# Performance work log

Hardware: AMD Instinct MI355X
Metric: run time of the kernel (lower is better)

Reference implementation:

```python
import jax, jax.numpy as jnp
import numpy as np

N_POINTS = 300000
N_PAIRS = 100000  # rulebook pairs per kernel offset
K_OFFSETS = 27    # 3x3x3 kernel
C_IN, C_OUT = 32, 64
GROUPS = 8
EPS = 1e-5
NEG_SLOPE = 0.01


def setup_inputs() -> dict:
    key = jax.random.key(0)
    k1, k2, k3, k4 = jax.random.split(key, 4)
    feats = jax.random.normal(k1, (N_POINTS, C_IN), dtype=jnp.float32)
    weight = jax.random.normal(k2, (K_OFFSETS, C_IN, C_OUT), dtype=jnp.float32) * (1.0 / np.sqrt(C_IN * K_OFFSETS))
    gamma = jnp.ones((C_OUT,), dtype=jnp.float32)
    beta = jnp.zeros((C_OUT,), dtype=jnp.float32)
    in_idx = jax.random.randint(k3, (K_OFFSETS, N_PAIRS), 0, N_POINTS, dtype=jnp.int64)
    out_idx = jax.random.randint(k4, (K_OFFSETS, N_PAIRS), 0, N_POINTS, dtype=jnp.int64)
    return {"feats": feats, "weight": weight, "gamma": gamma, "beta": beta,
            "in_idx": in_idx, "out_idx": out_idx}


def reference(feats, weight, gamma, beta, in_idx, out_idx):
    # Sparse 3D conv via rulebook: gather -> per-offset matmul -> scatter-add
    gathered = feats[in_idx]                       # [K, P, C_in]
    y = jnp.einsum('kpi,kio->kpo', gathered, weight)  # [K, P, C_out]
    out = jnp.zeros((feats.shape[0], weight.shape[2]), feats.dtype)
    out = out.at[out_idx.reshape(-1)].add(y.reshape(-1, weight.shape[2]))
    # GroupNorm(8, C_out): stats over all points and channels within each group
    N, C = out.shape
    xg = out.reshape(N, GROUPS, C // GROUPS)
    mean = jnp.mean(xg, axis=(0, 2), keepdims=True)
    var = jnp.var(xg, axis=(0, 2), keepdims=True)
    xn = ((xg - mean) * jax.lax.rsqrt(var + EPS)).reshape(N, C)
    xn = xn * gamma + beta
    # LeakyReLU (default negative_slope = 0.01)
    return jnp.where(xn >= 0, xn, NEG_SLOPE * xn)
```

## Files before the change

kernel.cpp:

```cpp
#include <hip/hip_runtime.h>

#define NPTS   300000
#define NPAIRS 100000
#define KOFF   27
#define CIN    32
#define COUT   64
#define NGROUP 8
#define EPSV   1e-5f
#define SLOPE  0.01f

#define PAIRS_PER_BLOCK 256
#define BLOCKS_PER_K ((NPAIRS + PAIRS_PER_BLOCK - 1) / PAIRS_PER_BLOCK)

__global__ __launch_bounds__(256) void zero_kernel(float4* __restrict__ out4, int n4,
                                                   float* __restrict__ stats) {
    int i = blockIdx.x * blockDim.x + threadIdx.x;
    if (i < n4) out4[i] = make_float4(0.f, 0.f, 0.f, 0.f);
    if (blockIdx.x == 0 && threadIdx.x < 16) stats[threadIdx.x] = 0.f;
}

__global__ __launch_bounds__(256) void conv_kernel(
    const float* __restrict__ feats, const float* __restrict__ weight,
    const int* __restrict__ in_idx, const int* __restrict__ out_idx,
    float* __restrict__ out)
{
    const int lane = threadIdx.x & 63;
    const int wave = threadIdx.x >> 6;
    const int k     = blockIdx.x / BLOCKS_PER_K;
    const int pair0 = (blockIdx.x % BLOCKS_PER_K) * PAIRS_PER_BLOCK;

    float w[CIN];
    const float* wk = weight + k * (CIN * COUT) + lane;
#pragma unroll
    for (int i = 0; i < CIN; ++i) w[i] = wk[i * COUT];

    const int per_wave = PAIRS_PER_BLOCK / 4;
    int p    = pair0 + wave * per_wave;
    int pend = p + per_wave;
    if (pend > NPAIRS) pend = NPAIRS;

    const int* ii = in_idx  + k * NPAIRS;
    const int* oi = out_idx + k * NPAIRS;

    for (; p < pend; ++p) {
        int rin  = __builtin_amdgcn_readfirstlane(ii[p]);
        int rout = __builtin_amdgcn_readfirstlane(oi[p]);
        const float* frow = feats + (size_t)rin * CIN;
        float acc = 0.f;
#pragma unroll
        for (int i = 0; i < CIN; ++i)
            acc = fmaf(frow[i], w[i], acc);
        atomicAdd(out + (size_t)rout * COUT + lane, acc);
    }
}

__global__ __launch_bounds__(256) void stats_kernel(const float* __restrict__ out,
                                                    float* __restrict__ stats) {
    const int c = threadIdx.x & 63;
    const int wave_in_grid = blockIdx.x * 4 + (threadIdx.x >> 6);
    const int nwaves = gridDim.x * 4;
    float s = 0.f, ss = 0.f;
    for (int r = wave_in_grid; r < NPTS; r += nwaves) {
        float v = out[(size_t)r * COUT + c];
        s += v; ss += v * v;
    }
#pragma unroll
    for (int m = 1; m < 8; m <<= 1) {
        s  += __shfl_xor(s,  m, 64);
        ss += __shfl_xor(ss, m, 64);
    }
    if ((c & 7) == 0) {
        int g = c >> 3;
        atomicAdd(stats + g,     s);
        atomicAdd(stats + 8 + g, ss);
    }
}

__global__ __launch_bounds__(256) void norm_kernel(float4* __restrict__ out4, int n4,
                                                   const float* __restrict__ stats,
                                                   const float* __restrict__ gamma,
                                                   const float* __restrict__ beta) {
    int i = blockIdx.x * blockDim.x + threadIdx.x;
    if (i >= n4) return;
    int c0 = (i & 15) * 4;
    int g  = c0 >> 3;
    const float cnt = (float)NPTS * (COUT / NGROUP);
    float mean = stats[g] / cnt;
    float var  = stats[8 + g] / cnt - mean * mean;
    float inv  = rsqrtf(var + EPSV);
    float4 v  = out4[i];
    float4 ga = *(const float4*)(gamma + c0);
    float4 be = *(const float4*)(beta  + c0);
    float x;
    x = (v.x - mean) * inv * ga.x + be.x; v.x = x >= 0.f ? x : SLOPE * x;
    x = (v.y - mean) * inv * ga.y + be.y; v.y = x >= 0.f ? x : SLOPE * x;
    x = (v.z - mean) * inv * ga.z + be.z; v.z = x >= 0.f ? x : SLOPE * x;
    x = (v.w - mean) * inv * ga.w + be.w; v.w = x >= 0.f ? x : SLOPE * x;
    out4[i] = v;
}

extern "C" void kernel_launch(void* const* d_in, const int* in_sizes, int n_in,
                              void* d_out, int out_size, void* d_ws, size_t ws_size,
                              hipStream_t stream) {
    const float* feats  = (const float*)d_in[0];
    const float* weight = (const float*)d_in[1];
    const float* gamma  = (const float*)d_in[2];
    const float* beta   = (const float*)d_in[3];
    const int*   in_idx = (const int*)d_in[4];
    const int*   out_idx= (const int*)d_in[5];
    float* out   = (float*)d_out;
    float* stats = (float*)d_ws;

    int n4 = out_size / 4;
    int zb = (n4 + 255) / 256;

    zero_kernel<<<zb, 256, 0, stream>>>((float4*)out, n4, stats);
    conv_kernel<<<KOFF * BLOCKS_PER_K, 256, 0, stream>>>(feats, weight, in_idx, out_idx, out);
    stats_kernel<<<1024, 256, 0, stream>>>(out, stats);
    norm_kernel<<<zb, 256, 0, stream>>>((float4*)out, n4, stats, gamma, beta);
}
```

Measured before the change: 821.7 us.

## Replace atomic scatter with counting-sort slots, bf16 features and per-row reduction

Builds a histogram and prefix scan over out_idx so that every pair gets its own slot in a row-sorted buffer. The conv kernel then writes bf16 partial results to those slots instead of doing float atomics, and a second kernel sums each output row without atomics. Features are also converted to bf16 to cut gather bandwidth. The price is several extra launches, a workspace of about 375 MB, and reduced precision in both the inputs and the partial sums. The old atomic path is kept as a fallback when the workspace is too small.

```diff
diff --git a/kernel.cpp b/kernel.cpp
--- a/kernel.cpp
+++ b/kernel.cpp
@@ -3,6 +3,7 @@
 #define NPTS   300000
 #define NPAIRS 100000
 #define KOFF   27
+#define NTOT   (KOFF * NPAIRS)
 #define CIN    32
 #define COUT   64
 #define NGROUP 8
@@ -12,17 +13,111 @@
 #define PAIRS_PER_BLOCK 256
 #define BLOCKS_PER_K ((NPAIRS + PAIRS_PER_BLOCK - 1) / PAIRS_PER_BLOCK)
 
-__global__ __launch_bounds__(256) void zero_kernel(float4* __restrict__ out4, int n4,
-                                                   float* __restrict__ stats) {
-    int i = blockIdx.x * blockDim.x + threadIdx.x;
-    if (i < n4) out4[i] = make_float4(0.f, 0.f, 0.f, 0.f);
+#define NB1 293
+
+#define OFS_STATS  0u
+#define OFS_CURSOR 4096u
+#define OFS_PART   (OFS_CURSOR + 1200128u)
+#define OFS_PSLOT  (OFS_PART + 8192u)
+#define OFS_SLOTS  (OFS_PSLOT + 10800128u)
+#define OFS_FB16   (OFS_SLOTS + 345600000u)
+#define WS_NEEDED  ((size_t)OFS_FB16 + 19200000u)
+
+__device__ inline unsigned short f2b(float x) {
+    unsigned u = __float_as_uint(x);
+    u += 0x7FFFu + ((u >> 16) & 1u);
+    return (unsigned short)(u >> 16);
+}
+__device__ inline float b2f_lo(unsigned d)  { return __uint_as_float(d << 16); }
+__device__ inline float b2f_hi(unsigned d)  { return __uint_as_float(d & 0xFFFF0000u); }
+
+
+__global__ __launch_bounds__(256) void to_bf16_kernel(const float2* __restrict__ src,
+                                                      unsigned* __restrict__ dst, int n2) {
+    int i = blockIdx.x * 256 + threadIdx.x;
+    if (i < n2) {
+        float2 v = src[i];
+        dst[i] = (unsigned)f2b(v.x) | ((unsigned)f2b(v.y) << 16);
+    }
+}
+
+__global__ __launch_bounds__(256) void zero_aux_kernel(int* __restrict__ cursor,
+                                                       float* __restrict__ stats) {
+    int i = blockIdx.x * 256 + threadIdx.x;
+    if (i < NPTS) cursor[i] = 0;
     if (blockIdx.x == 0 && threadIdx.x < 16) stats[threadIdx.x] = 0.f;
 }
 
-__global__ __launch_bounds__(256) void conv_kernel(
-    const float* __restrict__ feats, const float* __restrict__ weight,
-    const int* __restrict__ in_idx, const int* __restrict__ out_idx,
-    float* __restrict__ out)
+__global__ __launch_bounds__(256) void hist_kernel(const int* __restrict__ oi,
+                                                   int* __restrict__ cursor) {
+    int i = blockIdx.x * 256 + threadIdx.x;
+    if (i < NTOT) atomicAdd(cursor + oi[i], 1);
+}
+
+__global__ __launch_bounds__(256) void reduce_blocks_kernel(const int* __restrict__ cursor,
+                                                            int* __restrict__ part) {
+    __shared__ int sm[256];
+    int tid = threadIdx.x, i0 = blockIdx.x * 1024 + tid * 4;
+    int s = 0;
+#pragma unroll
+    for (int j = 0; j < 4; ++j) if (i0 + j < NPTS) s += cursor[i0 + j];
+    sm[tid] = s; __syncthreads();
+    for (int off = 128; off; off >>= 1) {
+        if (tid < off) sm[tid] += sm[tid + off];
+        __syncthreads();
+    }
+    if (tid == 0) part[blockIdx.x] = sm[0];
+}
+
+__global__ __launch_bounds__(512) void scan_partials_kernel(int* __restrict__ part) {
+    __shared__ int sm[512];
+    int tid = threadIdx.x;
+    int v = (tid < NB1) ? part[tid] : 0;
+    sm[tid] = v; __syncthreads();
+    for (int off = 1; off < 512; off <<= 1) {
+        int t = (tid >= off) ? sm[tid - off] : 0;
+        __syncthreads();
+        sm[tid] += t;
+        __syncthreads();
+    }
+    if (tid < NB1) part[tid] = sm[tid] - v;
+}
+
+__global__ __launch_bounds__(256) void scan_apply_kernel(int* __restrict__ cursor,
+                                                         const int* __restrict__ part) {
+    __shared__ int sm[256];
+    int tid = threadIdx.x, i0 = blockIdx.x * 1024 + tid * 4;
+    int c0 = 0, c1 = 0, c2 = 0, c3 = 0;
+    if (i0 + 0 < NPTS) c0 = cursor[i0 + 0];
+    if (i0 + 1 < NPTS) c1 = cursor[i0 + 1];
+    if (i0 + 2 < NPTS) c2 = cursor[i0 + 2];
+    if (i0 + 3 < NPTS) c3 = cursor[i0 + 3];
+    int s = c0 + c1 + c2 + c3;
+    sm[tid] = s; __syncthreads();
+    for (int off = 1; off < 256; off <<= 1) {
+        int t = (tid >= off) ? sm[tid - off] : 0;
+        __syncthreads();
+        sm[tid] += t;
+        __syncthreads();
+    }
+    int excl = sm[tid] - s + part[blockIdx.x];
+    if (i0 + 0 < NPTS) cursor[i0 + 0] = excl;
+    if (i0 + 1 < NPTS) cursor[i0 + 1] = excl + c0;
+    if (i0 + 2 < NPTS) cursor[i0 + 2] = excl + c0 + c1;
+    if (i0 + 3 < NPTS) cursor[i0 + 3] = excl + c0 + c1 + c2;
+}
+
+__global__ __launch_bounds__(256) void fill_kernel(const int* __restrict__ oi,
+                                                   int* __restrict__ cursor,
+                                                   int* __restrict__ pair_slot) {
+    int i = blockIdx.x * 256 + threadIdx.x;
+    if (i < NTOT) pair_slot[i] = atomicAdd(cursor + oi[i], 1);
+}
+
+__global__ __launch_bounds__(256) void convA_kernel(
+    const unsigned* __restrict__ fb16, const float* __restrict__ weight,
+    const int* __restrict__ in_idx, const int* __restrict__ pair_slot,
+    unsigned short* __restrict__ slots16)
 {
     const int lane = threadIdx.x & 63;
     const int wave = threadIdx.x >> 6;
@@ -39,19 +134,37 @@
     int pend = p + per_wave;
     if (pend > NPAIRS) pend = NPAIRS;
 
-    const int* ii = in_idx  + k * NPAIRS;
-    const int* oi = out_idx + k * NPAIRS;
+    const int* ii = in_idx    + k * NPAIRS;
+    const int* ps = pair_slot + k * NPAIRS;
 
     for (; p < pend; ++p) {
         int rin  = __builtin_amdgcn_readfirstlane(ii[p]);
-        int rout = __builtin_amdgcn_readfirstlane(oi[p]);
-        const float* frow = feats + (size_t)rin * CIN;
+        int slot = __builtin_amdgcn_readfirstlane(ps[p]);
+        const unsigned* fr = fb16 + rin * (CIN / 2);
         float acc = 0.f;
 #pragma unroll
-        for (int i = 0; i < CIN; ++i)
-            acc = fmaf(frow[i], w[i], acc);
-        atomicAdd(out + (size_t)rout * COUT + lane, acc);
-    }
+        for (int j = 0; j < CIN / 2; ++j) {
+            unsigned d = fr[j];
+            acc = fmaf(b2f_lo(d), w[2 * j],     acc);
+            acc = fmaf(b2f_hi(d), w[2 * j + 1], acc);
+        }
+        slots16[(size_t)slot * COUT + lane] = f2b(acc);
+    }
+}
+
+__global__ __launch_bounds__(256) void reduceB_kernel(const unsigned short* __restrict__ slots16,
+                                                      const int* __restrict__ ends,
+                                                      float* __restrict__ out)
+{
+    const int lane = threadIdx.x & 63;
+    const int row  = blockIdx.x * 4 + (threadIdx.x >> 6);
+    if (row >= NPTS) return;
+    int e = ends[row];
+    int s = (row == 0) ? 0 : ends[row - 1];
+    float acc = 0.f;
+    for (; s < e; ++s)
+        acc += __uint_as_float(((unsigned)slots16[(size_t)s * COUT + lane]) << 16);
+    out[(size_t)row * COUT + lane] = acc;
 }
 
 __global__ __launch_bounds__(256) void stats_kernel(const float* __restrict__ out,
@@ -99,23 +212,82 @@
     out4[i] = v;
 }
 
+__global__ __launch_bounds__(256) void zero_out_kernel(float4* __restrict__ out4, int n4,
+                                                       float* __restrict__ stats) {
+    int i = blockIdx.x * blockDim.x + threadIdx.x;
+    if (i < n4) out4[i] = make_float4(0.f, 0.f, 0.f, 0.f);
+    if (blockIdx.x == 0 && threadIdx.x < 16) stats[threadIdx.x] = 0.f;
+}
+
+__global__ __launch_bounds__(256) void conv_atomic_kernel(
+    const float* __restrict__ feats, const float* __restrict__ weight,
+    const int* __restrict__ in_idx, const int* __restrict__ out_idx,
+    float* __restrict__ out)
+{
+    const int lane = threadIdx.x & 63;
+    const int wave = threadIdx.x >> 6;
+    const int k     = blockIdx.x / BLOCKS_PER_K;
+    const int pair0 = (blockIdx.x % BLOCKS_PER_K) * PAIRS_PER_BLOCK;
+    float w[CIN];
+    const float* wk = weight + k * (CIN * COUT) + lane;
+#pragma unroll
+    for (int i = 0; i < CIN; ++i) w[i] = wk[i * COUT];
+    const int per_wave = PAIRS_PER_BLOCK / 4;
+    int p = pair0 + wave * per_wave;
+    int pend = p + per_wave;
+    if (pend > NPAIRS) pend = NPAIRS;
+    const int* ii = in_idx  + k * NPAIRS;
+    const int* oi = out_idx + k * NPAIRS;
+    for (; p < pend; ++p) {
+        int rin  = __builtin_amdgcn_readfirstlane(ii[p]);
+        int rout = __builtin_amdgcn_readfirstlane(oi[p]);
+        const float* frow = feats + (size_t)rin * CIN;
+        float acc = 0.f;
+#pragma unroll
+        for (int i = 0; i < CIN; ++i) acc = fmaf(frow[i], w[i], acc);
+        atomicAdd(out + (size_t)rout * COUT + lane, acc);
+    }
+}
+
 extern "C" void kernel_launch(void* const* d_in, const int* in_sizes, int n_in,
                               void* d_out, int out_size, void* d_ws, size_t ws_size,
                               hipStream_t stream) {
-    const float* feats  = (const float*)d_in[0];
-    const float* weight = (const float*)d_in[1];
-    const float* gamma  = (const float*)d_in[2];
-    const float* beta   = (const float*)d_in[3];
-    const int*   in_idx = (const int*)d_in[4];
-    const int*   out_idx= (const int*)d_in[5];
-    float* out   = (float*)d_out;
-    float* stats = (float*)d_ws;
+    const float* feats   = (const float*)d_in[0];
+    const float* weight  = (const float*)d_in[1];
+    const float* gamma   = (const float*)d_in[2];
+    const float* beta    = (const float*)d_in[3];
+    const int*   in_idx  = (const int*)d_in[4];
+    const int*   out_idx = (const int*)d_in[5];
+    float* out = (float*)d_out;
+
+    char* ws = (char*)d_ws;
+    float*          stats     = (float*)(ws + OFS_STATS);
+    int*            cursor    = (int*)(ws + OFS_CURSOR);
+    int*            part      = (int*)(ws + OFS_PART);
+    int*            pair_slot = (int*)(ws + OFS_PSLOT);
+    unsigned short* slots16   = (unsigned short*)(ws + OFS_SLOTS);
+    unsigned*       fb16      = (unsigned*)(ws + OFS_FB16);
 
     int n4 = out_size / 4;
     int zb = (n4 + 255) / 256;
 
-    zero_kernel<<<zb, 256, 0, stream>>>((float4*)out, n4, stats);
-    conv_kernel<<<KOFF * BLOCKS_PER_K, 256, 0, stream>>>(feats, weight, in_idx, out_idx, out);
-    stats_kernel<<<1024, 256, 0, stream>>>(out, stats);
-    norm_kernel<<<zb, 256, 0, stream>>>((float4*)out, n4, stats, gamma, beta);
-}
+    if (ws_size >= WS_NEEDED) {
+        int n2 = NPTS * CIN / 2;
+        to_bf16_kernel<<<(n2 + 255) / 256, 256, 0, stream>>>((const float2*)feats, fb16, n2);
+        zero_aux_kernel<<<(NPTS + 255) / 256, 256, 0, stream>>>(cursor, stats);
+        hist_kernel<<<(NTOT + 255) / 256, 256, 0, stream>>>(out_idx, cursor);
+        reduce_blocks_kernel<<<NB1, 256, 0, stream>>>(cursor, part);
+        scan_partials_kernel<<<1, 512, 0, stream>>>(part);
+        scan_apply_kernel<<<NB1, 256, 0, stream>>>(cursor, part);
+        fill_kernel<<<(NTOT + 255) / 256, 256, 0, stream>>>(out_idx, cursor, pair_slot);
+        convA_kernel<<<KOFF * BLOCKS_PER_K, 256, 0, stream>>>(fb16, weight, in_idx, pair_slot, slots16);
+        reduceB_kernel<<<(NPTS + 3) / 4, 256, 0, stream>>>(slots16, cursor, out);
+        stats_kernel<<<1024, 256, 0, stream>>>(out, stats);
+        norm_kernel<<<zb, 256, 0, stream>>>((float4*)out, n4, stats, gamma, beta);
+    } else {
+        zero_out_kernel<<<zb, 256, 0, stream>>>((float4*)out, n4, stats);
+        conv_atomic_kernel<<<KOFF * BLOCKS_PER_K, 256, 0, stream>>>(feats, weight, in_idx, out_idx, out);
+        stats_kernel<<<1024, 256, 0, stream>>>(out, stats);
+        norm_kernel<<<zb, 256, 0, stream>>>((float4*)out, n4, stats, gamma, beta);
+    }
+}
```

Result: no change. 823.8 us (+0.2%).

## Gather features from a bf16 copy in workspace and unroll conv loop

Applied to the files above, without the earlier changes.

Adds a pre-pass that converts input features to bf16 in workspace, and a conv kernel that gathers half-width rows and widens them to fp32 before the FMAs. The goal is to halve gather traffic in the conv, which is bound by random memory access. It also pins weight registers with asm, unrolls the pair loop by two and doubles the stats grid. The cost is an extra conversion pass and reduced input precision, which may break the accuracy tolerance. When the workspace is too small, the code falls back to the fp32 path.

```diff
diff --git a/kernel.cpp b/kernel.cpp
--- a/kernel.cpp
+++ b/kernel.cpp
@@ -3,6 +3,7 @@
 #define NPTS   300000
 #define NPAIRS 100000
 #define KOFF   27
+#define NTOT   (KOFF * NPAIRS)
 #define CIN    32
 #define COUT   64
 #define NGROUP 8
@@ -12,6 +13,18 @@
 #define PAIRS_PER_BLOCK 256
 #define BLOCKS_PER_K ((NPAIRS + PAIRS_PER_BLOCK - 1) / PAIRS_PER_BLOCK)
 
+#define OFS_STATS 0u
+#define OFS_FB16  4096u
+#define WS_BF16  ((size_t)OFS_FB16 + (size_t)NPTS * CIN * 2)
+
+__device__ inline unsigned short f2b(float x) {
+    unsigned u = __float_as_uint(x);
+    u += 0x7FFFu + ((u >> 16) & 1u);
+    return (unsigned short)(u >> 16);
+}
+__device__ inline float b2f_lo(unsigned d) { return __uint_as_float(d << 16); }
+__device__ inline float b2f_hi(unsigned d) { return __uint_as_float(d & 0xFFFF0000u); }
+
 __global__ __launch_bounds__(256) void zero_kernel(float4* __restrict__ out4, int n4,
                                                    float* __restrict__ stats) {
     int i = blockIdx.x * blockDim.x + threadIdx.x;
@@ -19,7 +32,57 @@
     if (blockIdx.x == 0 && threadIdx.x < 16) stats[threadIdx.x] = 0.f;
 }
 
-__global__ __launch_bounds__(256) void conv_kernel(
+__global__ __launch_bounds__(256) void to_bf16_kernel(const float2* __restrict__ src,
+                                                      unsigned* __restrict__ dst, int n2) {
+    int i = blockIdx.x * 256 + threadIdx.x;
+    if (i < n2) {
+        float2 v = src[i];
+        dst[i] = (unsigned)f2b(v.x) | ((unsigned)f2b(v.y) << 16);
+    }
+}
+
+__global__ __launch_bounds__(256) void conv_bf16_kernel(
+    const unsigned* __restrict__ fb16, const float* __restrict__ weight,
+    const int* __restrict__ in_idx, const int* __restrict__ out_idx,
+    float* __restrict__ out)
+{
+    const int lane = threadIdx.x & 63;
+    const int wave = threadIdx.x >> 6;
+    const int k     = blockIdx.x / BLOCKS_PER_K;
+    const int pair0 = (blockIdx.x % BLOCKS_PER_K) * PAIRS_PER_BLOCK;
+
+    float w[CIN];
+    const float* wk = weight + k * (CIN * COUT) + lane;
+#pragma unroll
+    for (int i = 0; i < CIN; ++i) w[i] = wk[i * COUT];
+#pragma unroll
+    for (int i = 0; i < CIN; ++i) asm volatile("" : "+v"(w[i]));
+
+    const int per_wave = PAIRS_PER_BLOCK / 4;
+    int p    = pair0 + wave * per_wave;
+    int pend = p + per_wave;
+    if (pend > NPAIRS) pend = NPAIRS;
+
+    const int* ii = in_idx  + k * NPAIRS;
+    const int* oi = out_idx + k * NPAIRS;
+
+#pragma unroll 2
+    for (; p < pend; ++p) {
+        int rin  = __builtin_amdgcn_readfirstlane(ii[p]);
+        int rout = __builtin_amdgcn_readfirstlane(oi[p]);
+        const unsigned* fr = fb16 + (size_t)rin * (CIN / 2);
+        float acc = 0.f;
+#pragma unroll
+        for (int j = 0; j < CIN / 2; ++j) {
+            unsigned d = fr[j];
+            acc = fmaf(b2f_lo(d), w[2 * j],     acc);
+            acc = fmaf(b2f_hi(d), w[2 * j + 1], acc);
+        }
+        atomicAdd(out + (size_t)rout * COUT + lane, acc);
+    }
+}
+
+__global__ __launch_bounds__(256) void conv_f32_kernel(
     const float* __restrict__ feats, const float* __restrict__ weight,
     const int* __restrict__ in_idx, const int* __restrict__ out_idx,
     float* __restrict__ out)
@@ -33,6 +96,8 @@
     const float* wk = weight + k * (CIN * COUT) + lane;
 #pragma unroll
     for (int i = 0; i < CIN; ++i) w[i] = wk[i * COUT];
+#pragma unroll
+    for (int i = 0; i < CIN; ++i) asm volatile("" : "+v"(w[i]));
 
     const int per_wave = PAIRS_PER_BLOCK / 4;
     int p    = pair0 + wave * per_wave;
@@ -42,6 +107,7 @@
     const int* ii = in_idx  + k * NPAIRS;
     const int* oi = out_idx + k * NPAIRS;
 
+#pragma unroll 2
     for (; p < pend; ++p) {
         int rin  = __builtin_amdgcn_readfirstlane(ii[p]);
         int rout = __builtin_amdgcn_readfirstlane(oi[p]);
@@ -102,20 +168,31 @@
 extern "C" void kernel_launch(void* const* d_in, const int* in_sizes, int n_in,
                               void* d_out, int out_size, void* d_ws, size_t ws_size,
                               hipStream_t stream) {
-    const float* feats  = (const float*)d_in[0];
-    const float* weight = (const float*)d_in[1];
-    const float* gamma  = (const float*)d_in[2];
-    const float* beta   = (const float*)d_in[3];
-    const int*   in_idx = (const int*)d_in[4];
-    const int*   out_idx= (const int*)d_in[5];
-    float* out   = (float*)d_out;
-    float* stats = (float*)d_ws;
+    const float* feats   = (const float*)d_in[0];
+    const float* weight  = (const float*)d_in[1];
+    const float* gamma   = (const float*)d_in[2];
+    const float* beta    = (const float*)d_in[3];
+    const int*   in_idx  = (const int*)d_in[4];
+    const int*   out_idx = (const int*)d_in[5];
+    float* out = (float*)d_out;
+
+    char* ws = (char*)d_ws;
+    float*    stats = (float*)(ws + OFS_STATS);
+    unsigned* fb16  = (unsigned*)(ws + OFS_FB16);
 
     int n4 = out_size / 4;
     int zb = (n4 + 255) / 256;
 
     zero_kernel<<<zb, 256, 0, stream>>>((float4*)out, n4, stats);
-    conv_kernel<<<KOFF * BLOCKS_PER_K, 256, 0, stream>>>(feats, weight, in_idx, out_idx, out);
-    stats_kernel<<<1024, 256, 0, stream>>>(out, stats);
+
+    if (ws_size >= WS_BF16) {
+        int n2 = NPTS * CIN / 2;
+        to_bf16_kernel<<<(n2 + 255) / 256, 256, 0, stream>>>((const float2*)feats, fb16, n2);
+        conv_bf16_kernel<<<KOFF * BLOCKS_PER_K, 256, 0, stream>>>(fb16, weight, in_idx, out_idx, out);
+    } else {
+        conv_f32_kernel<<<KOFF * BLOCKS_PER_K, 256, 0, stream>>>(feats, weight, in_idx, out_idx, out);
+    }
+
+    stats_kernel<<<2048, 256, 0, stream>>>(out, stats);
     norm_kernel<<<zb, 256, 0, stream>>>((float4*)out, n4, stats, gamma, beta);
 }
```

New measurement: 923.8 us. 1.12x slower.
